# Kernel optimization log

Measured on AMD Instinct MI355X. Metric: run time of the kernel, lower is better.

The kernel has to match this reference:

```python
import jax, jax.numpy as jnp
import numpy as np
import math

B, S, HID = 4, 2048, 1024
NH = 16
HD = HID // NH  # 64
DH = math.sqrt(HD)


def setup_inputs() -> dict:
    key = jax.random.key(0)
    ks = jax.random.split(key, 7)
    scale = 1.0 / math.sqrt(HID)
    return {
        "hidden_states": jax.random.normal(ks[0], (B, S, HID), dtype=jnp.float32),
        "Wq": jax.random.normal(ks[1], (HID, HID), dtype=jnp.float32) * scale,
        "bq": jnp.zeros((HID,), dtype=jnp.float32),
        "Wk": jax.random.normal(ks[2], (HID, HID), dtype=jnp.float32) * scale,
        "bk": jnp.zeros((HID,), dtype=jnp.float32),
        "Wv": jax.random.normal(ks[3], (HID, HID), dtype=jnp.float32) * scale,
        "bv": jnp.zeros((HID,), dtype=jnp.float32),
        "attention_mask": jnp.ones((B, S), dtype=jnp.int32),
    }


def _heads(x):
    # [B,S,HID] -> [B,NH,S,HD]
    b, s, _ = x.shape
    return x.reshape(b, s, NH, HD).transpose(0, 2, 1, 3)


def reference(hidden_states, Wq, bq, Wk, bk, Wv, bv, attention_mask):
    q = _heads(hidden_states @ Wq.T + bq)
    k = _heads(hidden_states @ Wk.T + bk)
    v = _heads(hidden_states @ Wv.T + bv)

    left_k = k / DH
    right_k = jax.nn.soft_sign(jax.nn.soft_sign(k) / DH) + v
    # scores: [B,NH,S,S]
    scores = jnp.einsum("bhqd,bhkd->bhqk", q, left_k + right_k) / DH
    # torch masks along the QUERY dim: mask[:, None, :, None] == 0 -> -10000
    scores = jnp.where(attention_mask[:, None, :, None] == 0, -10000.0, scores)
    probs = jax.nn.softmax(scores, axis=-1)
    ctx = jnp.einsum("bhqk,bhkd->bhqd", probs, v)
    # [B,NH,S,HD] -> [B,S,HID]
    return ctx.transpose(0, 2, 1, 3).reshape(hidden_states.shape[0], -1, HID)
```

## Files before the change

### kernel.cpp

```cpp
#include <hip/hip_runtime.h>
#include <hip/hip_fp16.h>
#include <cstdint>

#define B_   4
#define S_   2048
#define HID_ 1024
#define NH_  16
#define HD_  64
#define M_   (B_ * S_)

using f16   = _Float16;
using f16x4 = __attribute__((ext_vector_type(4))) _Float16;
using f16x8 = __attribute__((ext_vector_type(8))) _Float16;
using f32x4 = __attribute__((ext_vector_type(4))) float;
using u32x4 = __attribute__((ext_vector_type(4))) unsigned int;

__device__ __forceinline__ void g2lds16(const void* g, void* l) {
  __builtin_amdgcn_global_load_lds(
      (__attribute__((address_space(1))) void*)(uintptr_t)g,
      (__attribute__((address_space(3))) void*)(uint32_t)(uintptr_t)l,
      16, 0, 0);
}

__device__ __forceinline__ unsigned int pk16(float a, float b) {
  unsigned int r;
  asm("v_cvt_pkrtz_f16_f32 %0, %1, %2" : "=v"(r) : "v"(a), "v"(b));
  return r;
}

#define PIDX(r) (((r) & 32) | (((r) & 12) << 1) | ((((r) >> 4) & 1) << 2) | ((r) & 3))

__global__ void cvt_f32_f16_k(const float* __restrict__ src, f16* __restrict__ dst, int n4) {
  int i = blockIdx.x * blockDim.x + threadIdx.x;
  if (i >= n4) return;
  float4 v = ((const float4*)src)[i];
  f16x4 h;
  h[0] = (f16)v.x; h[1] = (f16)v.y; h[2] = (f16)v.z; h[3] = (f16)v.w;
  ((f16x4*)dst)[i] = h;
}

__global__ __launch_bounds__(256) void proj_gemm_k(
    const f16* __restrict__ A, const f16* __restrict__ W,
    const float* __restrict__ bq, const float* __restrict__ bk, const float* __restrict__ bv,
    f16* __restrict__ Out) {
  __shared__ __align__(16) f16 As[128 * 64];
  __shared__ __align__(16) f16 Bs[128 * 64];
  const int tid = threadIdx.x;
  const int l   = tid & 63;
  const int w   = tid >> 6;
  const int lr  = l & 15;
  const int lk  = (l >> 4) * 8;
  const int col0 = blockIdx.x * 128;
  const int row0 = blockIdx.y * 128;
  const int wr = (w >> 1) * 64;
  const int wc = (w & 1) * 64;

  f32x4 acc[4][4] = {};

  for (int kt = 0; kt < 16; ++kt) {
    const int k0 = kt * 64;
#pragma unroll
    for (int i = 0; i < 4; ++i) {
      const int c   = tid + i * 256;
      const int row = c >> 3;
      const int cb  = (c ^ row) & 7;
      g2lds16(A + (size_t)(row0 + row) * 1024 + k0 + cb * 8,
              As + (w * 64 + i * 256) * 8);
      g2lds16(W + (size_t)(col0 + row) * 1024 + k0 + cb * 8,
              Bs + (w * 64 + i * 256) * 8);
    }
    asm volatile("s_waitcnt vmcnt(0)" ::: "memory");
    __syncthreads();

#pragma unroll
    for (int kk = 0; kk < 64; kk += 32) {
      const int x = (kk + lk) >> 3;
      f16x8 af[4], bf[4];
#pragma unroll
      for (int m = 0; m < 4; ++m) {
        const int row = wr + m * 16 + lr;
        af[m] = *(const f16x8*)(As + (row * 8 + ((x ^ row) & 7)) * 8);
      }
#pragma unroll
      for (int n = 0; n < 4; ++n) {
        const int row = wc + n * 16 + lr;
        bf[n] = *(const f16x8*)(Bs + (row * 8 + ((x ^ row) & 7)) * 8);
      }
#pragma unroll
      for (int m = 0; m < 4; ++m)
#pragma unroll
        for (int n = 0; n < 4; ++n)
          acc[m][n] = __builtin_amdgcn_mfma_f32_16x16x32_f16(af[m], bf[n], acc[m][n], 0, 0, 0);
    }
    __syncthreads();
  }

  const int proj = col0 >> 10;
  const float* bias = (proj == 0) ? bq : ((proj == 1) ? bk : bv);
  f16* outp = Out + (size_t)proj * ((size_t)M_ * HID_);
#pragma unroll
  for (int n = 0; n < 4; ++n) {
    const int col = col0 + wc + n * 16 + lr;
    const int cp  = col & 1023;
    const float bb = bias[cp];
#pragma unroll
    for (int m = 0; m < 4; ++m) {
      const int rbase = row0 + wr + m * 16 + (l >> 4) * 4;
#pragma unroll
      for (int r = 0; r < 4; ++r)
        outp[(size_t)(rbase + r) * 1024 + cp] = (f16)(acc[m][n][r] + bb);
    }
  }
}

__global__ __launch_bounds__(256) void prep_kv_k(
    const f16* __restrict__ Kp, const f16* __restrict__ Vp,
    f16* __restrict__ Keff, f16* __restrict__ Vt) {
  const int bh = blockIdx.x;
  const int st = blockIdx.y;
  const int b = bh >> 4, h = bh & 15;
  const int tid = threadIdx.x;
  const float Cs = 0.180336880111120426f;
#pragma unroll
  for (int i = 0; i < 2; ++i) {
    const int c  = tid + i * 256;
    const int sl = c >> 3, cb = c & 7;
    const int s  = st * 64 + sl;
    const size_t src = (size_t)(b * S_ + s) * 1024 + h * 64 + cb * 8;
    const f16x8 kv = *(const f16x8*)(Kp + src);
    const f16x8 vv = *(const f16x8*)(Vp + src);
    f16x8 ke;
#pragma unroll
    for (int j = 0; j < 8; ++j) {
      const float kf = (float)kv[j], vf = (float)vv[j];
      const float s1 = kf / (1.f + fabsf(kf));
      const float t  = s1 * 0.125f;
      const float s2 = t / (1.f + fabsf(t));
      ke[j] = (f16)((kf * 0.125f + s2 + vf) * Cs);
    }
    *(f16x8*)(Keff + ((size_t)bh * S_ + s) * 64 + cb * 8) = ke;
#pragma unroll
    for (int j = 0; j < 8; ++j)
      Vt[((size_t)bh * 64 + cb * 8 + j) * S_ + s] = vv[j];
  }
}

__global__ __launch_bounds__(512) void attn_k(
    const f16* __restrict__ Q,
    const f16* __restrict__ Keff,
    const f16* __restrict__ Vt,
    const int* __restrict__ mask,
    float* __restrict__ Out) {
  __shared__ __align__(16) f16 Kl[2][64 * 64];
  __shared__ __align__(16) f16 Vl[2][64 * 64];
  const int bh = blockIdx.x, qt = blockIdx.y;
  const int b = bh >> 4, h = bh & 15;
  const int tid = threadIdx.x;
  const int l = tid & 63, w = tid >> 6;
  const int lr = l & 15, g = l >> 4;

  f16x8 qf[4][2];
#pragma unroll
  for (int qb = 0; qb < 4; ++qb) {
    const int qrow = qt * 512 + w * 64 + qb * 16 + lr;
    const f16* qs = Q + (size_t)(b * S_ + qrow) * 1024 + h * 64 + g * 8;
    qf[qb][0] = *(const f16x8*)(qs);
    qf[qb][1] = *(const f16x8*)(qs + 32);
    if (mask[b * S_ + qrow] == 0) {
      qf[qb][0] = (f16x8)(f16)0;
      qf[qb][1] = (f16x8)(f16)0;
    }
  }

  const int srow = tid >> 3, scl = tid & 7;
  const int sc = scl ^ (srow & 7);
  const f16* kg = Keff + ((size_t)bh * S_ + PIDX(srow)) * 64 + sc * 8;
  const f16* vg = Vt + ((size_t)bh * 64 + srow) * 2048 + sc * 8;

  f32x4 ctx[4][4] = {};
  float lacc[4] = {0.f, 0.f, 0.f, 0.f};

#define STAGE(bf, t)                                                           \
  {                                                                            \
    g2lds16(kg + (size_t)(t) * 4096, &Kl[bf][(w * 64) * 8]);                   \
    g2lds16(vg + (size_t)(t) * 64, &Vl[bf][(w * 64) * 8]);                     \
  }

  STAGE(0, 0);
  asm volatile("s_waitcnt vmcnt(0)" ::: "memory");
  __syncthreads();

  for (int kt = 0; kt < 32; ++kt) {
    const int cur = kt & 1;
    if (kt < 31) STAGE(cur ^ 1, kt + 1);

    f16x8 pf[4][2];
#pragma unroll
    for (int cbp = 0; cbp < 2; ++cbp) {
      f32x4 sv[4][2] = {};
      __builtin_amdgcn_s_setprio(1);
#pragma unroll
      for (int kk = 0; kk < 2; ++kk)
#pragma unroll
        for (int cc = 0; cc < 2; ++cc) {
          const int row = (cbp * 2 + cc) * 16 + lr;
          const f16x8 kf = *(const f16x8*)(&Kl[cur][(row * 8 + ((kk * 4 + g) ^ (row & 7))) * 8]);
#pragma unroll
          for (int qb = 0; qb < 4; ++qb)
            sv[qb][cc] = __builtin_amdgcn_mfma_f32_16x16x32_f16(kf, qf[qb][kk], sv[qb][cc], 0, 0, 0);
        }
      __builtin_amdgcn_s_setprio(0);
#pragma unroll
      for (int qb = 0; qb < 4; ++qb) {
        float pv[2][4];
        float s = 0.f;
#pragma unroll
        for (int cc = 0; cc < 2; ++cc)
#pragma unroll
          for (int r = 0; r < 4; ++r) {
            const float pe = __builtin_amdgcn_exp2f(sv[qb][cc][r]);
            pv[cc][r] = pe;
            s += pe;
          }
        lacc[qb] += s;
        u32x4 pw = {pk16(pv[0][0], pv[0][1]), pk16(pv[0][2], pv[0][3]),
                    pk16(pv[1][0], pv[1][1]), pk16(pv[1][2], pv[1][3])};
        pf[qb][cbp] = __builtin_bit_cast(f16x8, pw);
      }
    }

    __builtin_amdgcn_s_setprio(1);
#pragma unroll
    for (int kk = 0; kk < 2; ++kk)
#pragma unroll
      for (int db = 0; db < 4; ++db) {
        const int row = db * 16 + lr;
        const f16x8 vf = *(const f16x8*)(&Vl[cur][(row * 8 + ((kk * 4 + g) ^ (row & 7))) * 8]);
#pragma unroll
        for (int qb = 0; qb < 4; ++qb)
          ctx[qb][db] = __builtin_amdgcn_mfma_f32_16x16x32_f16(vf, pf[qb][kk], ctx[qb][db], 0, 0, 0);
      }
    __builtin_amdgcn_s_setprio(0);

    asm volatile("s_waitcnt vmcnt(0)" ::: "memory");
    __syncthreads();
  }

#pragma unroll
  for (int qb = 0; qb < 4; ++qb) {
    float ls = lacc[qb];
    ls += __shfl_xor(ls, 16);
    ls += __shfl_xor(ls, 32);
    const float linv = 1.0f / ls;
    const int qrow = qt * 512 + w * 64 + qb * 16 + lr;
    float* op = Out + (size_t)(b * S_ + qrow) * 1024 + h * 64 + g * 4;
#pragma unroll
    for (int db = 0; db < 4; ++db) {
      f32x4 o = ctx[qb][db] * linv;
      *(f32x4*)(op + db * 16) = o;
    }
  }
}

extern "C" void kernel_launch(void* const* d_in, const int* in_sizes, int n_in,
                              void* d_out, int out_size, void* d_ws, size_t ws_size,
                              hipStream_t stream) {
  const float* hs = (const float*)d_in[0];
  const float* Wq = (const float*)d_in[1];
  const float* bq = (const float*)d_in[2];
  const float* Wk = (const float*)d_in[3];
  const float* bk = (const float*)d_in[4];
  const float* Wv = (const float*)d_in[5];
  const float* bv = (const float*)d_in[6];
  const int* mask = (const int*)d_in[7];
  float* out = (float*)d_out;

  f16* hsF  = (f16*)d_ws;
  f16* wF   = hsF + (size_t)M_ * HID_;
  f16* qF   = wF + 3ull * HID_ * HID_;
  f16* kF   = qF + (size_t)M_ * HID_;
  f16* vF   = kF + (size_t)M_ * HID_;
  f16* keff = vF + (size_t)M_ * HID_;
  f16* vt   = keff + (size_t)M_ * HID_;

  cvt_f32_f16_k<<<dim3((M_ * HID_) / 1024), 256, 0, stream>>>(hs, hsF, (M_ * HID_) / 4);
  cvt_f32_f16_k<<<dim3((HID_ * HID_) / 1024), 256, 0, stream>>>(Wq, wF, (HID_ * HID_) / 4);
  cvt_f32_f16_k<<<dim3((HID_ * HID_) / 1024), 256, 0, stream>>>(Wk, wF + (size_t)HID_ * HID_, (HID_ * HID_) / 4);
  cvt_f32_f16_k<<<dim3((HID_ * HID_) / 1024), 256, 0, stream>>>(Wv, wF + 2ull * (size_t)HID_ * HID_, (HID_ * HID_) / 4);

  proj_gemm_k<<<dim3(24, 64), 256, 0, stream>>>(hsF, wF, bq, bk, bv, qF);
  prep_kv_k<<<dim3(64, 32), 256, 0, stream>>>(kF, vF, keff, vt);
  attn_k<<<dim3(64, 4), 512, 0, stream>>>(qF, keff, vt, mask, out);
}
```

Before: 168.3 us.

## Fuse K/V projection with Keff/Vt prep and halve attention query tile

Splits the combined QKV projection into a Q-only GEMM and a K+V GEMM that computes both projections sharing the A tile. The K+V epilogue applies the softsign-based Keff transform and writes transposed V directly, removing the separate prep kernel and its round trip of K/V through global memory. The attention kernel now processes 256 query rows per block instead of 512, doubling the grid to 512 blocks for better CU occupancy. The cost is that K/V tiles are re-streamed twice as often, the fused GEMM uses more registers and LDS, and the epilogue does scattered Keff/Vt stores.

```diff
diff --git a/kernel.cpp b/kernel.cpp
--- a/kernel.cpp
+++ b/kernel.cpp
@@ -29,6 +29,8 @@
 }
 
 #define PIDX(r) (((r) & 32) | (((r) & 12) << 1) | ((((r) >> 4) & 1) << 2) | ((r) & 3))
+
+#define CS_ 0.180336880111120426f
 
 __global__ void cvt_f32_f16_k(const float* __restrict__ src, f16* __restrict__ dst, int n4) {
   int i = blockIdx.x * blockDim.x + threadIdx.x;
@@ -39,10 +41,9 @@
   ((f16x4*)dst)[i] = h;
 }
 
-__global__ __launch_bounds__(256) void proj_gemm_k(
+__global__ __launch_bounds__(256) void proj_q_k(
     const f16* __restrict__ A, const f16* __restrict__ W,
-    const float* __restrict__ bq, const float* __restrict__ bk, const float* __restrict__ bv,
-    f16* __restrict__ Out) {
+    const float* __restrict__ bq, f16* __restrict__ Out) {
   __shared__ __align__(16) f16 As[128 * 64];
   __shared__ __align__(16) f16 Bs[128 * 64];
   const int tid = threadIdx.x;
@@ -95,53 +96,107 @@
     __syncthreads();
   }
 
-  const int proj = col0 >> 10;
-  const float* bias = (proj == 0) ? bq : ((proj == 1) ? bk : bv);
-  f16* outp = Out + (size_t)proj * ((size_t)M_ * HID_);
 #pragma unroll
   for (int n = 0; n < 4; ++n) {
-    const int col = col0 + wc + n * 16 + lr;
-    const int cp  = col & 1023;
-    const float bb = bias[cp];
+    const int cp = col0 + wc + n * 16 + lr;
+    const float bb = bq[cp];
 #pragma unroll
     for (int m = 0; m < 4; ++m) {
       const int rbase = row0 + wr + m * 16 + (l >> 4) * 4;
 #pragma unroll
       for (int r = 0; r < 4; ++r)
-        outp[(size_t)(rbase + r) * 1024 + cp] = (f16)(acc[m][n][r] + bb);
-    }
-  }
-}
-
-__global__ __launch_bounds__(256) void prep_kv_k(
-    const f16* __restrict__ Kp, const f16* __restrict__ Vp,
+        Out[(size_t)(rbase + r) * 1024 + cp] = (f16)(acc[m][n][r] + bb);
+    }
+  }
+}
+
+__global__ __launch_bounds__(256) void proj_kv_k(
+    const f16* __restrict__ A, const f16* __restrict__ Wk_, const f16* __restrict__ Wv_,
+    const float* __restrict__ bk, const float* __restrict__ bv,
     f16* __restrict__ Keff, f16* __restrict__ Vt) {
-  const int bh = blockIdx.x;
-  const int st = blockIdx.y;
-  const int b = bh >> 4, h = bh & 15;
+  __shared__ __align__(16) f16 As[128 * 64];
+  __shared__ __align__(16) f16 Bk[128 * 64];
+  __shared__ __align__(16) f16 Bv[128 * 64];
   const int tid = threadIdx.x;
-  const float Cs = 0.180336880111120426f;
-#pragma unroll
-  for (int i = 0; i < 2; ++i) {
-    const int c  = tid + i * 256;
-    const int sl = c >> 3, cb = c & 7;
-    const int s  = st * 64 + sl;
-    const size_t src = (size_t)(b * S_ + s) * 1024 + h * 64 + cb * 8;
-    const f16x8 kv = *(const f16x8*)(Kp + src);
-    const f16x8 vv = *(const f16x8*)(Vp + src);
-    f16x8 ke;
-#pragma unroll
-    for (int j = 0; j < 8; ++j) {
-      const float kf = (float)kv[j], vf = (float)vv[j];
-      const float s1 = kf / (1.f + fabsf(kf));
-      const float t  = s1 * 0.125f;
-      const float s2 = t / (1.f + fabsf(t));
-      ke[j] = (f16)((kf * 0.125f + s2 + vf) * Cs);
-    }
-    *(f16x8*)(Keff + ((size_t)bh * S_ + s) * 64 + cb * 8) = ke;
-#pragma unroll
-    for (int j = 0; j < 8; ++j)
-      Vt[((size_t)bh * 64 + cb * 8 + j) * S_ + s] = vv[j];
+  const int l   = tid & 63;
+  const int w   = tid >> 6;
+  const int lr  = l & 15;
+  const int lk  = (l >> 4) * 8;
+  const int col0 = blockIdx.x * 128;
+  const int row0 = blockIdx.y * 128;
+  const int wr = (w >> 1) * 64;
+  const int wc = (w & 1) * 64;
+
+  f32x4 kacc[4][4] = {};
+  f32x4 vacc[4][4] = {};
+
+  for (int kt = 0; kt < 16; ++kt) {
+    const int k0 = kt * 64;
+#pragma unroll
+    for (int i = 0; i < 4; ++i) {
+      const int c   = tid + i * 256;
+      const int row = c >> 3;
+      const int cb  = (c ^ row) & 7;
+      g2lds16(A + (size_t)(row0 + row) * 1024 + k0 + cb * 8,
+              As + (w * 64 + i * 256) * 8);
+      g2lds16(Wk_ + (size_t)(col0 + row) * 1024 + k0 + cb * 8,
+              Bk + (w * 64 + i * 256) * 8);
+      g2lds16(Wv_ + (size_t)(col0 + row) * 1024 + k0 + cb * 8,
+              Bv + (w * 64 + i * 256) * 8);
+    }
+    asm volatile("s_waitcnt vmcnt(0)" ::: "memory");
+    __syncthreads();
+
+#pragma unroll
+    for (int kk = 0; kk < 64; kk += 32) {
+      const int x = (kk + lk) >> 3;
+      f16x8 af[4], bkf[4], bvf[4];
+#pragma unroll
+      for (int m = 0; m < 4; ++m) {
+        const int row = wr + m * 16 + lr;
+        af[m] = *(const f16x8*)(As + (row * 8 + ((x ^ row) & 7)) * 8);
+      }
+#pragma unroll
+      for (int n = 0; n < 4; ++n) {
+        const int row = wc + n * 16 + lr;
+        bkf[n] = *(const f16x8*)(Bk + (row * 8 + ((x ^ row) & 7)) * 8);
+        bvf[n] = *(const f16x8*)(Bv + (row * 8 + ((x ^ row) & 7)) * 8);
+      }
+#pragma unroll
+      for (int m = 0; m < 4; ++m)
+#pragma unroll
+        for (int n = 0; n < 4; ++n) {
+          kacc[m][n] = __builtin_amdgcn_mfma_f32_16x16x32_f16(af[m], bkf[n], kacc[m][n], 0, 0, 0);
+          vacc[m][n] = __builtin_amdgcn_mfma_f32_16x16x32_f16(af[m], bvf[n], vacc[m][n], 0, 0, 0);
+        }
+    }
+    __syncthreads();
+  }
+
+#pragma unroll
+  for (int n = 0; n < 4; ++n) {
+    const int cp = col0 + wc + n * 16 + lr;
+    const int h = cp >> 6, d = cp & 63;
+    const float bbk = bk[cp], bbv = bv[cp];
+#pragma unroll
+    for (int m = 0; m < 4; ++m) {
+      const int rbase = row0 + wr + m * 16 + (l >> 4) * 4;
+      const int b = rbase >> 11;
+      const int s0 = rbase & 2047;
+      const size_t bh64 = (size_t)(b * 16 + h);
+      f16x4 vv4;
+#pragma unroll
+      for (int r = 0; r < 4; ++r) {
+        const float kf = kacc[m][n][r] + bbk;
+        const float vf = vacc[m][n][r] + bbv;
+        const float s1 = kf / (1.f + fabsf(kf));
+        const float t  = s1 * 0.125f;
+        const float s2 = t / (1.f + fabsf(t));
+        Keff[(bh64 * S_ + s0 + r) * 64 + d] = (f16)((kf * 0.125f + s2 + vf) * CS_);
+        vv4[r] = (f16)vf;
+      }
+      *(f16x4*)(&Vt[(bh64 * 64 + d) * S_ + s0]) = vv4;
+    }
   }
 }
 
@@ -159,10 +214,10 @@
   const int l = tid & 63, w = tid >> 6;
   const int lr = l & 15, g = l >> 4;
 
-  f16x8 qf[4][2];
-#pragma unroll
-  for (int qb = 0; qb < 4; ++qb) {
-    const int qrow = qt * 512 + w * 64 + qb * 16 + lr;
+  f16x8 qf[2][2];
+#pragma unroll
+  for (int qb = 0; qb < 2; ++qb) {
+    const int qrow = qt * 256 + w * 32 + qb * 16 + lr;
     const f16* qs = Q + (size_t)(b * S_ + qrow) * 1024 + h * 64 + g * 8;
     qf[qb][0] = *(const f16x8*)(qs);
     qf[qb][1] = *(const f16x8*)(qs + 32);
@@ -177,8 +232,8 @@
   const f16* kg = Keff + ((size_t)bh * S_ + PIDX(srow)) * 64 + sc * 8;
   const f16* vg = Vt + ((size_t)bh * 64 + srow) * 2048 + sc * 8;
 
-  f32x4 ctx[4][4] = {};
-  float lacc[4] = {0.f, 0.f, 0.f, 0.f};
+  f32x4 ctx[2][4] = {};
+  float lacc[2] = {0.f, 0.f};
 
 #define STAGE(bf, t)                                                           \
   {                                                                            \
@@ -194,10 +249,10 @@
     const int cur = kt & 1;
     if (kt < 31) STAGE(cur ^ 1, kt + 1);
 
-    f16x8 pf[4][2];
+    f16x8 pf[2][2];
 #pragma unroll
     for (int cbp = 0; cbp < 2; ++cbp) {
-      f32x4 sv[4][2] = {};
+      f32x4 sv[2][2] = {};
       __builtin_amdgcn_s_setprio(1);
 #pragma unroll
       for (int kk = 0; kk < 2; ++kk)
@@ -206,12 +261,12 @@
           const int row = (cbp * 2 + cc) * 16 + lr;
           const f16x8 kf = *(const f16x8*)(&Kl[cur][(row * 8 + ((kk * 4 + g) ^ (row & 7))) * 8]);
 #pragma unroll
-          for (int qb = 0; qb < 4; ++qb)
+          for (int qb = 0; qb < 2; ++qb)
             sv[qb][cc] = __builtin_amdgcn_mfma_f32_16x16x32_f16(kf, qf[qb][kk], sv[qb][cc], 0, 0, 0);
         }
       __builtin_amdgcn_s_setprio(0);
 #pragma unroll
-      for (int qb = 0; qb < 4; ++qb) {
+      for (int qb = 0; qb < 2; ++qb) {
         float pv[2][4];
         float s = 0.f;
 #pragma unroll
@@ -237,7 +292,7 @@
         const int row = db * 16 + lr;
         const f16x8 vf = *(const f16x8*)(&Vl[cur][(row * 8 + ((kk * 4 + g) ^ (row & 7))) * 8]);
 #pragma unroll
-        for (int qb = 0; qb < 4; ++qb)
+        for (int qb = 0; qb < 2; ++qb)
           ctx[qb][db] = __builtin_amdgcn_mfma_f32_16x16x32_f16(vf, pf[qb][kk], ctx[qb][db], 0, 0, 0);
       }
     __builtin_amdgcn_s_setprio(0);
@@ -247,12 +302,12 @@
   }
 
 #pragma unroll
-  for (int qb = 0; qb < 4; ++qb) {
+  for (int qb = 0; qb < 2; ++qb) {
     float ls = lacc[qb];
     ls += __shfl_xor(ls, 16);
     ls += __shfl_xor(ls, 32);
     const float linv = 1.0f / ls;
-    const int qrow = qt * 512 + w * 64 + qb * 16 + lr;
+    const int qrow = qt * 256 + w * 32 + qb * 16 + lr;
     float* op = Out + (size_t)(b * S_ + qrow) * 1024 + h * 64 + g * 4;
 #pragma unroll
     for (int db = 0; db < 4; ++db) {
@@ -278,9 +333,7 @@
   f16* hsF  = (f16*)d_ws;
   f16* wF   = hsF + (size_t)M_ * HID_;
   f16* qF   = wF + 3ull * HID_ * HID_;
-  f16* kF   = qF + (size_t)M_ * HID_;
-  f16* vF   = kF + (size_t)M_ * HID_;
-  f16* keff = vF + (size_t)M_ * HID_;
+  f16* keff = qF + (size_t)M_ * HID_;
   f16* vt   = keff + (size_t)M_ * HID_;
 
   cvt_f32_f16_k<<<dim3((M_ * HID_) / 1024), 256, 0, stream>>>(hs, hsF, (M_ * HID_) / 4);
@@ -288,7 +341,8 @@
   cvt_f32_f16_k<<<dim3((HID_ * HID_) / 1024), 256, 0, stream>>>(Wk, wF + (size_t)HID_ * HID_, (HID_ * HID_) / 4);
   cvt_f32_f16_k<<<dim3((HID_ * HID_) / 1024), 256, 0, stream>>>(Wv, wF + 2ull * (size_t)HID_ * HID_, (HID_ * HID_) / 4);
 
-  proj_gemm_k<<<dim3(24, 64), 256, 0, stream>>>(hsF, wF, bq, bk, bv, qF);
-  prep_kv_k<<<dim3(64, 32), 256, 0, stream>>>(kF, vF, keff, vt);
-  attn_k<<<dim3(64, 4), 512, 0, stream>>>(qF, keff, vt, mask, out);
-}
+  proj_q_k<<<dim3(8, 64), 256, 0, stream>>>(hsF, wF, bq, qF);
+  proj_kv_k<<<dim3(8, 64), 256, 0, stream>>>(hsF, wF + (size_t)HID_ * HID_,
+                                             wF + 2ull * (size_t)HID_ * HID_, bk, bv, keff, vt);
+  attn_k<<<dim3(64, 8), 512, 0, stream>>>(qF, keff, vt, mask, out);
+}
```

Result: slower. 182.3 us (+8.4%).
